# Kernel tuning notes

Measured on AMD Instinct MI355X. Metric: run time of the kernel, lower is better.

## Reference

```python
import jax, jax.numpy as jnp
import numpy as np

D_MODEL = 2048
D_HEAD = 64
Q_HEADS = 32
KV_HEADS = 8


def rope(x):
    # x: [B, S, H, D], rotate interleaved pairs along last dim
    B, S, H, D = x.shape
    pos = jnp.arange(S, dtype=x.dtype)
    freq = 1.0 / (10000.0 ** (jnp.arange(0, D, 2, dtype=x.dtype) / D))  # [D/2]
    theta = pos[:, None] * freq[None, :]                                 # [S, D/2]
    cos = jnp.cos(theta)[None, :, None, :]
    sin = jnp.sin(theta)[None, :, None, :]
    xr = x.reshape(B, S, H, D // 2, 2)
    x1, x2 = xr[..., 0], xr[..., 1]
    out = jnp.stack((x1 * cos - x2 * sin, x1 * sin + x2 * cos), axis=-1)
    return out.reshape(B, S, H, D)


def setup_inputs() -> dict:
    key = jax.random.key(0)
    ks = jax.random.split(key, 7)
    x = jax.random.normal(ks[0], (1, 2048, D_MODEL), dtype=jnp.float32)
    W_q = jax.random.normal(ks[1], (Q_HEADS * D_HEAD, D_MODEL), dtype=jnp.float32) * 0.02
    b_q = jnp.zeros((Q_HEADS * D_HEAD,), dtype=jnp.float32)
    W_kv = jax.random.normal(ks[2], (2 * KV_HEADS * D_HEAD, D_MODEL), dtype=jnp.float32) * 0.02
    b_kv = jnp.zeros((2 * KV_HEADS * D_HEAD,), dtype=jnp.float32)
    W_out = jax.random.normal(ks[3], (D_MODEL, D_MODEL), dtype=jnp.float32) * 0.02
    b_out = jnp.zeros((D_MODEL,), dtype=jnp.float32)
    return {"x": x, "W_q": W_q, "b_q": b_q, "W_kv": W_kv, "b_kv": b_kv,
            "W_out": W_out, "b_out": b_out}


def reference(x, W_q, b_q, W_kv, b_kv, W_out, b_out):
    B, S, _ = x.shape
    g = Q_HEADS // KV_HEADS
    Q = (x @ W_q.T + b_q).reshape(B, S, Q_HEADS, D_HEAD)
    kv = x @ W_kv.T + b_kv
    K, V = jnp.split(kv, 2, axis=-1)
    K = K.reshape(B, S, KV_HEADS, D_HEAD)
    V = V.reshape(B, S, KV_HEADS, D_HEAD)
    Q = rope(Q)
    K = rope(K)
    K = jnp.repeat(K, g, axis=2)  # [B, S, Q_HEADS, D_HEAD]
    V = jnp.repeat(V, g, axis=2)
    scale = 1.0 / (D_HEAD ** 0.5)
    scores = jnp.einsum('bqhd,bkhd->bhqk', Q, K) * scale  # [B,H,S,S]
    # note: original calls non-inplace masked_fill and discards it, so no causal mask applied
    probs = jax.nn.softmax(scores, axis=-1)
    attn = jnp.einsum('bhqk,bkhd->bqhd', probs, V).reshape(B, S, D_MODEL)
    return attn @ W_out.T + b_out
```

## Files before the change

### kernel.cpp

```cpp
#include <hip/hip_runtime.h>
#include <hip/hip_bf16.h>
#include <math.h>

#define S_LEN 2048
#define D_MODEL 2048
#define Q_HEADS 32
#define KV_HEADS 8

typedef __attribute__((ext_vector_type(8))) short short8;
typedef __attribute__((ext_vector_type(4))) float f32x4;

__device__ __forceinline__ short bf16_rne(float f) {
  unsigned u = __float_as_uint(f);
  unsigned r = (u + 0x7FFFu + ((u >> 16) & 1u)) >> 16;
  return (short)r;
}
__device__ __forceinline__ void dma16(const short* g, short* l) {
  __builtin_amdgcn_global_load_lds(
      (const __attribute__((address_space(1))) void*)g,
      (__attribute__((address_space(3))) void*)l, 16, 0, 0);
}
__device__ __forceinline__ void fast_sincos(float theta, float& sn, float& cs) {
  double rev = (double)theta * 0.15915494309189535;
  float fr = (float)(rev - floor(rev));
  sn = __builtin_amdgcn_sinf(fr);
  cs = __builtin_amdgcn_cosf(fr);
}
__device__ __forceinline__ void cvt8(const float* src, short* dst, int i) {
  float4 a = *(const float4*)&src[i];
  float4 b = *(const float4*)&src[i + 4];
  short8 h;
  h[0] = bf16_rne(a.x); h[1] = bf16_rne(a.y);
  h[2] = bf16_rne(a.z); h[3] = bf16_rne(a.w);
  h[4] = bf16_rne(b.x); h[5] = bf16_rne(b.y);
  h[6] = bf16_rne(b.z); h[7] = bf16_rne(b.w);
  *(short8*)&dst[i] = h;
}

#define NM (2048 * 2048)
#define NKV (1024 * 2048)

__global__ __launch_bounds__(256) void cvt_all(
    const float* __restrict__ x,    short* __restrict__ xh,
    const float* __restrict__ wq,   short* __restrict__ wqh,
    const float* __restrict__ wkv,  short* __restrict__ wkvh,
    const float* __restrict__ wo,   short* __restrict__ woh,
    float* __restrict__ freqTab) {
  if (blockIdx.x == 0 && threadIdx.x < 32) {
    const double e = (2.0 * threadIdx.x) / 64.0;
    freqTab[threadIdx.x] = (float)pow(10000.0, -e);
  }
  int i = (blockIdx.x * 256 + threadIdx.x) * 8;
  if (i < NM) { cvt8(x, xh, i); return; }
  i -= NM;
  if (i < NM) { cvt8(wq, wqh, i); return; }
  i -= NM;
  if (i < NKV) { cvt8(wkv, wkvh, i); return; }
  i -= NKV;
  cvt8(wo, woh, i);
}

__global__ __launch_bounds__(256) void gemm_nt1_dual(
    const short* __restrict__ Ah,
    const short* __restrict__ Bq, const short* __restrict__ Bkv,
    const float* __restrict__ bq, const float* __restrict__ bkv,
    float* __restrict__ Cq, float* __restrict__ Ckv,
    int Nq, int Nkv, int K) {
  __shared__ short As[2][128 * 32];
  __shared__ short Bs[2][64 * 32];
  const int tid = threadIdx.x;
  const int w = tid >> 6, lane = tid & 63;
  const int l16 = lane & 15, quad = lane >> 4;
  const int bm = blockIdx.y * 128;
  const int bnG = blockIdx.x * 64;

  const short* Bsrc; const float* bias; float* Cp; int pitch; int bn;
  if (bnG < Nq) { Bsrc = Bq;  bias = bq;  Cp = Cq;  pitch = Nq;  bn = bnG; }
  else          { Bsrc = Bkv; bias = bkv; Cp = Ckv; pitch = Nkv; bn = bnG - Nq; }

  const int drow0 = w * 16 + (lane >> 2);
  const int drow1 = drow0 + 64;
  const int slot = lane & 3;
  const int ch0 = slot ^ ((drow0 >> 1) & 3);
  const int ch1 = slot ^ ((drow1 >> 1) & 3);
  const size_t a0 = (size_t)(bm + drow0) * K + ch0 * 8;
  const size_t a1 = (size_t)(bm + drow1) * K + ch1 * 8;
  const size_t b0 = (size_t)(bn + drow0) * K + ch0 * 8;
  const int dA0 = (w * 16) * 32, dA1 = (64 + w * 16) * 32;

  const int wm = (w & 1) * 64, wn = (w >> 1) * 32;
  int offA[4], offB[2];
#pragma unroll
  for (int i = 0; i < 4; ++i) {
    int R = wm + i * 16 + l16;
    offA[i] = R * 32 + (quad ^ ((R >> 1) & 3)) * 8;
  }
#pragma unroll
  for (int j = 0; j < 2; ++j) {
    int R = wn + j * 16 + l16;
    offB[j] = R * 32 + (quad ^ ((R >> 1) & 3)) * 8;
  }

  f32x4 acc[4][2];
#pragma unroll
  for (int i = 0; i < 4; ++i)
#pragma unroll
    for (int j = 0; j < 2; ++j)
#pragma unroll
      for (int e = 0; e < 4; ++e) acc[i][j][e] = 0.f;

  const int T = K / 32;
  dma16(Ah + a0, &As[0][dA0]);
  dma16(Ah + a1, &As[0][dA1]);
  dma16(Bsrc + b0, &Bs[0][dA0]);
  __syncthreads();

  for (int t = 0; t < T; ++t) {
    const int cur = t & 1, nxt = cur ^ 1;
    if (t + 1 < T) {
      const int ko = (t + 1) * 32;
      dma16(Ah + a0 + ko, &As[nxt][dA0]);
      dma16(Ah + a1 + ko, &As[nxt][dA1]);
      dma16(Bsrc + b0 + ko, &Bs[nxt][dA0]);
    }
    short8 af[4], bf[2];
#pragma unroll
    for (int i = 0; i < 4; ++i) af[i] = *(const short8*)&As[cur][offA[i]];
#pragma unroll
    for (int j = 0; j < 2; ++j) bf[j] = *(const short8*)&Bs[cur][offB[j]];
#pragma unroll
    for (int i = 0; i < 4; ++i)
#pragma unroll
      for (int j = 0; j < 2; ++j)
        acc[i][j] = __builtin_amdgcn_mfma_f32_16x16x32_bf16(af[i], bf[j], acc[i][j], 0, 0, 0);
    __syncthreads();
  }

#pragma unroll
  for (int i = 0; i < 4; ++i) {
#pragma unroll
    for (int j = 0; j < 2; ++j) {
      const int col = bn + wn + j * 16 + l16;
      const float bv = bias[col];
      const int row0 = bm + wm + i * 16 + quad * 4;
#pragma unroll
      for (int e = 0; e < 4; ++e)
        Cp[(size_t)(row0 + e) * pitch + col] = acc[i][j][e] + bv;
    }
  }
}

__global__ __launch_bounds__(256) void gemm_nt1_big(
    const short* __restrict__ A, const short* __restrict__ B,
    const float* __restrict__ bias, float* __restrict__ C,
    int N, int K) {
  __shared__ short As[2][128 * 32];
  __shared__ short Bs[2][128 * 32];
  const int tid = threadIdx.x;
  const int w = tid >> 6, lane = tid & 63;
  const int l16 = lane & 15, quad = lane >> 4;
  const int bm = blockIdx.y * 128;
  const int bn = blockIdx.x * 128;

  const int drow0 = w * 16 + (lane >> 2);
  const int drow1 = drow0 + 64;
  const int slot = lane & 3;
  const int ch0 = slot ^ ((drow0 >> 1) & 3);
  const int ch1 = slot ^ ((drow1 >> 1) & 3);
  const short* gA0 = &A[(size_t)(bm + drow0) * K + ch0 * 8];
  const short* gA1 = &A[(size_t)(bm + drow1) * K + ch1 * 8];
  const short* gB0 = &B[(size_t)(bn + drow0) * K + ch0 * 8];
  const short* gB1 = &B[(size_t)(bn + drow1) * K + ch1 * 8];
  const int dA0 = (w * 16) * 32, dA1 = (64 + w * 16) * 32;

  const int wm = (w & 1) * 64, wn = (w >> 1) * 64;
  int offA[4], offB[4];
#pragma unroll
  for (int i = 0; i < 4; ++i) {
    int R = wm + i * 16 + l16;
    offA[i] = R * 32 + (quad ^ ((R >> 1) & 3)) * 8;
    int Rb = wn + i * 16 + l16;
    offB[i] = Rb * 32 + (quad ^ ((Rb >> 1) & 3)) * 8;
  }

  f32x4 acc[4][4];
#pragma unroll
  for (int i = 0; i < 4; ++i)
#pragma unroll
    for (int j = 0; j < 4; ++j)
#pragma unroll
      for (int e = 0; e < 4; ++e) acc[i][j][e] = 0.f;

  const int T = K / 32;
  dma16(gA0, &As[0][dA0]);
  dma16(gA1, &As[0][dA1]);
  dma16(gB0, &Bs[0][dA0]);
  dma16(gB1, &Bs[0][dA1]);
  __syncthreads();

  for (int t = 0; t < T; ++t) {
    const int cur = t & 1, nxt = cur ^ 1;
    if (t + 1 < T) {
      const int ko = (t + 1) * 32;
      dma16(gA0 + ko, &As[nxt][dA0]);
      dma16(gA1 + ko, &As[nxt][dA1]);
      dma16(gB0 + ko, &Bs[nxt][dA0]);
      dma16(gB1 + ko, &Bs[nxt][dA1]);
    }
    short8 af[4], bf[4];
#pragma unroll
    for (int i = 0; i < 4; ++i) af[i] = *(const short8*)&As[cur][offA[i]];
#pragma unroll
    for (int j = 0; j < 4; ++j) bf[j] = *(const short8*)&Bs[cur][offB[j]];
#pragma unroll
    for (int i = 0; i < 4; ++i)
#pragma unroll
      for (int j = 0; j < 4; ++j)
        acc[i][j] = __builtin_amdgcn_mfma_f32_16x16x32_bf16(af[i], bf[j], acc[i][j], 0, 0, 0);
    __syncthreads();
  }

#pragma unroll
  for (int i = 0; i < 4; ++i) {
#pragma unroll
    for (int j = 0; j < 4; ++j) {
      const int col = bn + wn + j * 16 + l16;
      const float bv = bias[col];
      const int row0 = bm + wm + i * 16 + quad * 4;
#pragma unroll
      for (int e = 0; e < 4; ++e)
        C[(size_t)(row0 + e) * N + col] = acc[i][j][e] + bv;
    }
  }
}

#define QSCALE 0.18033688011112042f

__global__ __launch_bounds__(256) void rope_all(
    const float* __restrict__ Qf, const float* __restrict__ KVf,
    const float* __restrict__ tab, short* __restrict__ Qb,
    short* __restrict__ Kb, short* __restrict__ Vt) {
  __shared__ short Vtile[64][72];
  const int tid = threadIdx.x;

  if (blockIdx.x < 8192) {
    const int g = blockIdx.x * 256 + tid;
    const int s = g >> 10;
    const int rem = g & 1023;
    const int h = rem >> 5, j = rem & 31;
    const float theta = (float)s * tab[j];
    float sn, cs;
    fast_sincos(theta, sn, cs);
    const float* p = &Qf[(size_t)s * D_MODEL + h * 64 + 2 * j];
    const float x1 = p[0], x2 = p[1];
    short2 o;
    o.x = bf16_rne((x1 * cs - x2 * sn) * QSCALE);
    o.y = bf16_rne((x1 * sn + x2 * cs) * QSCALE);
    *(short2*)&Qb[((size_t)h * S_LEN + s) * 64 + 2 * j] = o;
    return;
  }

  const int bb = blockIdx.x - 8192;
  const int st = bb & 31, kvh = bb >> 5;

  {
    const int sr = tid >> 2, sc = (tid & 3) * 16;
    const int s = st * 64 + sr;
    const float* kg = &KVf[(size_t)s * 1024 + kvh * 64 + sc];
    short tmp[16];
#pragma unroll
    for (int i = 0; i < 8; ++i) {
      const int j = (sc >> 1) + i;
      const float theta = (float)s * tab[j];
      float sn, cs;
      fast_sincos(theta, sn, cs);
      const float x1 = kg[2 * i], x2 = kg[2 * i + 1];
      tmp[2 * i]     = bf16_rne(x1 * cs - x2 * sn);
      tmp[2 * i + 1] = bf16_rne(x1 * sn + x2 * cs);
    }
    short* out = &Kb[((size_t)kvh * S_LEN + s) * 64 + sc];
    *(short8*)&out[0] = *(short8*)&tmp[0];
    *(short8*)&out[8] = *(short8*)&tmp[8];
  }

  {
    const int sr = tid >> 2, sc = (tid & 3) * 16;
    const float* vg = &KVf[(size_t)(st * 64 + sr) * 1024 + 512 + kvh * 64 + sc];
    short tmp[16];
#pragma unroll
    for (int c = 0; c < 16; c += 4) {
      float4 v = *(const float4*)&vg[c];
      tmp[c + 0] = bf16_rne(v.x);
      tmp[c + 1] = bf16_rne(v.y);
      tmp[c + 2] = bf16_rne(v.z);
      tmp[c + 3] = bf16_rne(v.w);
    }
    *(short8*)&Vtile[sr][sc]     = *(short8*)&tmp[0];
    *(short8*)&Vtile[sr][sc + 8] = *(short8*)&tmp[8];
  }
  __syncthreads();
  {
    const int d = tid & 63, kchunk = tid >> 6;
    short tmp[16];
#pragma unroll
    for (int k = 0; k < 16; ++k) tmp[k] = Vtile[kchunk * 16 + k][d];
    short* out = &Vt[((size_t)kvh * 64 + d) * S_LEN + st * 64 + kchunk * 16];
    *(short8*)&out[0] = *(short8*)&tmp[0];
    *(short8*)&out[8] = *(short8*)&tmp[8];
  }
}

__global__ __launch_bounds__(256, 4) void flash8(
    const short* __restrict__ Qb, const short* __restrict__ Kb,
    const short* __restrict__ Vt, short* __restrict__ Oh) {
  const int qt = blockIdx.x, h = blockIdx.y;
  const int kvh = h >> 2;
  const int tid = threadIdx.x;
  const int w = tid >> 6, lane = tid & 63;
  const int l16 = lane & 15, quad = lane >> 4;

  __shared__ short Ks[2][64 * 64];
  __shared__ short Vs[2][64 * 64];
  __shared__ short Ps[64 * 64];

  const short* Kh = Kb + (size_t)kvh * S_LEN * 64;
  const short* Vh = Vt + (size_t)kvh * 64 * S_LEN;
  const int qr = qt * 64 + w * 16 + l16;

  short8 qf0 = *(const short8*)&Qb[((size_t)h * S_LEN + qr) * 64 + quad * 8];
  short8 qf1 = *(const short8*)&Qb[((size_t)h * S_LEN + qr) * 64 + 32 + quad * 8];

  short8 ones;
#pragma unroll
  for (int e = 0; e < 8; ++e) ones[e] = (short)0x3F80;

  const int drow = lane >> 3;
  const int ch = (lane & 7) ^ drow;
  const short* gK = &Kh[(size_t)(w * 16 + drow) * 64 + ch * 8];
  const short* gV = &Vh[(size_t)(w * 16 + drow) * S_LEN + ch * 8];

  const int sl0 = quad ^ (l16 & 7);
  int offT[4][2];
#pragma unroll
  for (int m = 0; m < 4; ++m) {
    offT[m][0] = (m * 16 + l16) * 64 + sl0 * 8;
    offT[m][1] = (m * 16 + l16) * 64 + (sl0 ^ 4) * 8;
  }

  const int prow = (w * 16 + l16) * 64;
  const int pswz = (l16 & 7) << 1;
  int pwr[4];
#pragma unroll
  for (int m = 0; m < 4; ++m) pwr[m] = prow + ((4 * m + quad) ^ pswz) * 4;
  const int prd0 = prow + ((2 * quad) ^ pswz) * 4;
  const int prd1 = prow + ((8 + 2 * quad) ^ pswz) * 4;

  f32x4 accl;
#pragma unroll
  for (int e = 0; e < 4; ++e) accl[e] = 0.f;
  f32x4 acco[4];
#pragma unroll
  for (int m = 0; m < 4; ++m)
#pragma unroll
    for (int e = 0; e < 4; ++e) acco[m][e] = 0.f;

  dma16(gK,               &Ks[0][(w * 16) * 64]);
  dma16(gK + 8 * 64,      &Ks[0][(w * 16 + 8) * 64]);
  dma16(gV,               &Vs[0][(w * 16) * 64]);
  dma16(gV + 8 * S_LEN,   &Vs[0][(w * 16 + 8) * 64]);
  __syncthreads();

  for (int t = 0; t < 32; ++t) {
    const int cur = t & 1, nxt = cur ^ 1;
    if (t + 1 < 32) {
      const short* gKn = gK + (t + 1) * 4096;
      const short* gVn = gV + (t + 1) * 64;
      dma16(gKn,             &Ks[nxt][(w * 16) * 64]);
      dma16(gKn + 8 * 64,    &Ks[nxt][(w * 16 + 8) * 64]);
      dma16(gVn,             &Vs[nxt][(w * 16) * 64]);
      dma16(gVn + 8 * S_LEN, &Vs[nxt][(w * 16 + 8) * 64]);
    }

    const short* kc = Ks[cur];
    f32x4 accs[4];
#pragma unroll
    for (int m = 0; m < 4; ++m)
#pragma unroll
      for (int e = 0; e < 4; ++e) accs[m][e] = 0.f;
#pragma unroll
    for (int m = 0; m < 4; ++m) {
      short8 k0 = *(const short8*)&kc[offT[m][0]];
      short8 k1 = *(const short8*)&kc[offT[m][1]];
      accs[m] = __builtin_amdgcn_mfma_f32_16x16x32_bf16(k0, qf0, accs[m], 0, 0, 0);
      accs[m] = __builtin_amdgcn_mfma_f32_16x16x32_bf16(k1, qf1, accs[m], 0, 0, 0);
    }

#pragma unroll
    for (int m = 0; m < 4; ++m) {
      float p0 = exp2f(accs[m][0]);
      float p1 = exp2f(accs[m][1]);
      float p2 = exp2f(accs[m][2]);
      float p3 = exp2f(accs[m][3]);
      unsigned u01 = __builtin_amdgcn_perm(__float_as_uint(p1), __float_as_uint(p0), 0x07060302u);
      unsigned u23 = __builtin_amdgcn_perm(__float_as_uint(p3), __float_as_uint(p2), 0x07060302u);
      *(uint2*)&Ps[pwr[m]] = make_uint2(u01, u23);
    }

    short8 pf0 = *(const short8*)&Ps[prd0];
    short8 pf1 = *(const short8*)&Ps[prd1];
    accl = __builtin_amdgcn_mfma_f32_16x16x32_bf16(ones, pf0, accl, 0, 0, 0);
    accl = __builtin_amdgcn_mfma_f32_16x16x32_bf16(ones, pf1, accl, 0, 0, 0);
    const short* vc = Vs[cur];
#pragma unroll
    for (int m = 0; m < 4; ++m) {
      short8 v0 = *(const short8*)&vc[offT[m][0]];
      short8 v1 = *(const short8*)&vc[offT[m][1]];
      acco[m] = __builtin_amdgcn_mfma_f32_16x16x32_bf16(v0, pf0, acco[m], 0, 0, 0);
      acco[m] = __builtin_amdgcn_mfma_f32_16x16x32_bf16(v1, pf1, acco[m], 0, 0, 0);
    }

    __syncthreads();
  }

  const float inv = 1.f / accl[0];
#pragma unroll
  for (int m = 0; m < 4; ++m) {
    short4 h4;
    h4.x = bf16_rne(acco[m][0] * inv);
    h4.y = bf16_rne(acco[m][1] * inv);
    h4.z = bf16_rne(acco[m][2] * inv);
    h4.w = bf16_rne(acco[m][3] * inv);
    const size_t base = (size_t)qr * D_MODEL + h * 64 + m * 16 + quad * 4;
    *(short4*)&Oh[base] = h4;
  }
}

extern "C" void kernel_launch(void* const* d_in, const int* in_sizes, int n_in,
                              void* d_out, int out_size, void* d_ws, size_t ws_size,
                              hipStream_t stream) {
  const float* x     = (const float*)d_in[0];
  const float* W_q   = (const float*)d_in[1];
  const float* b_q   = (const float*)d_in[2];
  const float* W_kv  = (const float*)d_in[3];
  const float* b_kv  = (const float*)d_in[4];
  const float* W_out = (const float*)d_in[5];
  const float* b_out = (const float*)d_in[6];
  float* out = (float*)d_out;

  char* ws = (char*)d_ws;
  float* Qbuf  = (float*)(ws);
  float* KVbuf = (float*)(ws + (16u << 20));
  short* xh    = (short*)(ws + (24u << 20));
  short* Wqh   = (short*)(ws + (32u << 20));
  short* Wkvh  = (short*)(ws + (40u << 20));
  short* Woh   = (short*)(ws + (44u << 20));
  short* Qb    = (short*)(ws + (52u << 20));
  short* Kb    = (short*)(ws + (60u << 20));
  short* Vtb   = (short*)(ws + (62u << 20));
  float* freqTab = (float*)(ws + (64u << 20));
  short* Ath   = xh;

  cvt_all<<<7168, 256, 0, stream>>>(x, xh, W_q, Wqh, W_kv, Wkvh, W_out, Woh,
                                    freqTab);

  gemm_nt1_dual<<<dim3(3072 / 64, 2048 / 128), 256, 0, stream>>>(
      xh, Wqh, Wkvh, b_q, b_kv, Qbuf, KVbuf, 2048, 1024, 2048);

  rope_all<<<8192 + 256, 256, 0, stream>>>(Qbuf, KVbuf, freqTab, Qb, Kb, Vtb);

  flash8<<<dim3(S_LEN / 64, Q_HEADS), 256, 0, stream>>>(Qb, Kb, Vtb, Ath);

  gemm_nt1_big<<<dim3(2048 / 128, 2048 / 128), 256, 0, stream>>>(
      Ath, Woh, b_out, out, 2048, 2048);
}
```

Baseline: 264.2 us.

## Fuse RoPE, scaling, bf16 cast and V transpose into QKV GEMM epilogue

Removes the separate rope_all kernel and the fp32 Q/KV intermediates by applying RoPE, the Q scale and bf16 rounding directly in the QKV GEMM epilogue. Rotation partners are exchanged with a lane shuffle, and V is written transposed straight from the accumulators. The flash kernel now reads Q and K in row-major [S, heads*64] layout with strided addressing. This saves one launch and a large fp32 write/read round trip, in exchange for scattered short4 and scalar bf16 stores in the epilogue and less contiguous K loads in attention.

Result: no change. 261.7 us (-1.0%).

```diff
diff --git a/kernel.cpp b/kernel.cpp
--- a/kernel.cpp
+++ b/kernel.cpp
@@ -60,12 +60,16 @@
   cvt8(wo, woh, i);
 }
 
-__global__ __launch_bounds__(256) void gemm_nt1_dual(
+#define QSCALE 0.18033688011112042f
+
+__global__ __launch_bounds__(256) void gemm_qkv_rope(
     const short* __restrict__ Ah,
     const short* __restrict__ Bq, const short* __restrict__ Bkv,
     const float* __restrict__ bq, const float* __restrict__ bkv,
-    float* __restrict__ Cq, float* __restrict__ Ckv,
-    int Nq, int Nkv, int K) {
+    const float* __restrict__ tab,
+    short* __restrict__ Qrm, short* __restrict__ Krm,
+    short* __restrict__ Vt) {
+  const int Nq = 2048, K = 2048;
   __shared__ short As[2][128 * 32];
   __shared__ short Bs[2][64 * 32];
   const int tid = threadIdx.x;
@@ -74,9 +78,10 @@
   const int bm = blockIdx.y * 128;
   const int bnG = blockIdx.x * 64;
 
-  const short* Bsrc; const float* bias; float* Cp; int pitch; int bn;
-  if (bnG < Nq) { Bsrc = Bq;  bias = bq;  Cp = Cq;  pitch = Nq;  bn = bnG; }
-  else          { Bsrc = Bkv; bias = bkv; Cp = Ckv; pitch = Nkv; bn = bnG - Nq; }
+  const short* Bsrc; const float* bias; int bn;
+  if (bnG < Nq) { Bsrc = Bq;  bias = bq;  bn = bnG; }
+  else          { Bsrc = Bkv; bias = bkv; bn = bnG - Nq; }
+  const int mode = (bnG < Nq) ? 0 : ((bnG < Nq + 512) ? 1 : 2);
 
   const int drow0 = w * 16 + (lane >> 2);
   const int drow1 = drow0 + 64;
@@ -138,14 +143,35 @@
 
 #pragma unroll
   for (int i = 0; i < 4; ++i) {
+    const int row0 = bm + wm + i * 16 + quad * 4;
 #pragma unroll
     for (int j = 0; j < 2; ++j) {
       const int col = bn + wn + j * 16 + l16;
       const float bv = bias[col];
-      const int row0 = bm + wm + i * 16 + quad * 4;
-#pragma unroll
-      for (int e = 0; e < 4; ++e)
-        Cp[(size_t)(row0 + e) * pitch + col] = acc[i][j][e] + bv;
+      if (mode == 2) {
+        const int d = col - 512;
+        short4 sv;
+        sv.x = bf16_rne(acc[i][j][0] + bv);
+        sv.y = bf16_rne(acc[i][j][1] + bv);
+        sv.z = bf16_rne(acc[i][j][2] + bv);
+        sv.w = bf16_rne(acc[i][j][3] + bv);
+        *(short4*)&Vt[(size_t)d * S_LEN + row0] = sv;
+      } else {
+        const float fr = tab[(col & 63) >> 1];
+        const float sgn = (col & 1) ? 1.f : -1.f;
+#pragma unroll
+        for (int e = 0; e < 4; ++e) {
+          float v = acc[i][j][e] + bv;
+          float other = __shfl_xor(v, 1);
+          float sn, cs;
+          fast_sincos((float)(row0 + e) * fr, sn, cs);
+          const float o = v * cs + sgn * other * sn;
+          if (mode == 0)
+            Qrm[(size_t)(row0 + e) * D_MODEL + col] = bf16_rne(o * QSCALE);
+          else
+            Krm[(size_t)(row0 + e) * 512 + col] = bf16_rne(o);
+        }
+      }
     }
   }
 }
@@ -234,84 +260,8 @@
   }
 }
 
-#define QSCALE 0.18033688011112042f
-
-__global__ __launch_bounds__(256) void rope_all(
-    const float* __restrict__ Qf, const float* __restrict__ KVf,
-    const float* __restrict__ tab, short* __restrict__ Qb,
-    short* __restrict__ Kb, short* __restrict__ Vt) {
-  __shared__ short Vtile[64][72];
-  const int tid = threadIdx.x;
-
-  if (blockIdx.x < 8192) {
-    const int g = blockIdx.x * 256 + tid;
-    const int s = g >> 10;
-    const int rem = g & 1023;
-    const int h = rem >> 5, j = rem & 31;
-    const float theta = (float)s * tab[j];
-    float sn, cs;
-    fast_sincos(theta, sn, cs);
-    const float* p = &Qf[(size_t)s * D_MODEL + h * 64 + 2 * j];
-    const float x1 = p[0], x2 = p[1];
-    short2 o;
-    o.x = bf16_rne((x1 * cs - x2 * sn) * QSCALE);
-    o.y = bf16_rne((x1 * sn + x2 * cs) * QSCALE);
-    *(short2*)&Qb[((size_t)h * S_LEN + s) * 64 + 2 * j] = o;
-    return;
-  }
-
-  const int bb = blockIdx.x - 8192;
-  const int st = bb & 31, kvh = bb >> 5;
-
-  {
-    const int sr = tid >> 2, sc = (tid & 3) * 16;
-    const int s = st * 64 + sr;
-    const float* kg = &KVf[(size_t)s * 1024 + kvh * 64 + sc];
-    short tmp[16];
-#pragma unroll
-    for (int i = 0; i < 8; ++i) {
-      const int j = (sc >> 1) + i;
-      const float theta = (float)s * tab[j];
-      float sn, cs;
-      fast_sincos(theta, sn, cs);
-      const float x1 = kg[2 * i], x2 = kg[2 * i + 1];
-      tmp[2 * i]     = bf16_rne(x1 * cs - x2 * sn);
-      tmp[2 * i + 1] = bf16_rne(x1 * sn + x2 * cs);
-    }
-    short* out = &Kb[((size_t)kvh * S_LEN + s) * 64 + sc];
-    *(short8*)&out[0] = *(short8*)&tmp[0];
-    *(short8*)&out[8] = *(short8*)&tmp[8];
-  }
-
-  {
-    const int sr = tid >> 2, sc = (tid & 3) * 16;
-    const float* vg = &KVf[(size_t)(st * 64 + sr) * 1024 + 512 + kvh * 64 + sc];
-    short tmp[16];
-#pragma unroll
-    for (int c = 0; c < 16; c += 4) {
-      float4 v = *(const float4*)&vg[c];
-      tmp[c + 0] = bf16_rne(v.x);
-      tmp[c + 1] = bf16_rne(v.y);
-      tmp[c + 2] = bf16_rne(v.z);
-      tmp[c + 3] = bf16_rne(v.w);
-    }
-    *(short8*)&Vtile[sr][sc]     = *(short8*)&tmp[0];
-    *(short8*)&Vtile[sr][sc + 8] = *(short8*)&tmp[8];
-  }
-  __syncthreads();
-  {
-    const int d = tid & 63, kchunk = tid >> 6;
-    short tmp[16];
-#pragma unroll
-    for (int k = 0; k < 16; ++k) tmp[k] = Vtile[kchunk * 16 + k][d];
-    short* out = &Vt[((size_t)kvh * 64 + d) * S_LEN + st * 64 + kchunk * 16];
-    *(short8*)&out[0] = *(short8*)&tmp[0];
-    *(short8*)&out[8] = *(short8*)&tmp[8];
-  }
-}
-
 __global__ __launch_bounds__(256, 4) void flash8(
-    const short* __restrict__ Qb, const short* __restrict__ Kb,
+    const short* __restrict__ Qrm, const short* __restrict__ Krm,
     const short* __restrict__ Vt, short* __restrict__ Oh) {
   const int qt = blockIdx.x, h = blockIdx.y;
   const int kvh = h >> 2;
@@ -323,12 +273,11 @@
   __shared__ short Vs[2][64 * 64];
   __shared__ short Ps[64 * 64];
 
-  const short* Kh = Kb + (size_t)kvh * S_LEN * 64;
   const short* Vh = Vt + (size_t)kvh * 64 * S_LEN;
   const int qr = qt * 64 + w * 16 + l16;
 
-  short8 qf0 = *(const short8*)&Qb[((size_t)h * S_LEN + qr) * 64 + quad * 8];
-  short8 qf1 = *(const short8*)&Qb[((size_t)h * S_LEN + qr) * 64 + 32 + quad * 8];
+  short8 qf0 = *(const short8*)&Qrm[(size_t)qr * D_MODEL + h * 64 + quad * 8];
+  short8 qf1 = *(const short8*)&Qrm[(size_t)qr * D_MODEL + h * 64 + 32 + quad * 8];
 
   short8 ones;
 #pragma unroll
@@ -336,7 +285,7 @@
 
   const int drow = lane >> 3;
   const int ch = (lane & 7) ^ drow;
-  const short* gK = &Kh[(size_t)(w * 16 + drow) * 64 + ch * 8];
+  const short* gK = &Krm[(size_t)(w * 16 + drow) * 512 + kvh * 64 + ch * 8];
   const short* gV = &Vh[(size_t)(w * 16 + drow) * S_LEN + ch * 8];
 
   const int sl0 = quad ^ (l16 & 7);
@@ -365,7 +314,7 @@
     for (int e = 0; e < 4; ++e) acco[m][e] = 0.f;
 
   dma16(gK,               &Ks[0][(w * 16) * 64]);
-  dma16(gK + 8 * 64,      &Ks[0][(w * 16 + 8) * 64]);
+  dma16(gK + 8 * 512,     &Ks[0][(w * 16 + 8) * 64]);
   dma16(gV,               &Vs[0][(w * 16) * 64]);
   dma16(gV + 8 * S_LEN,   &Vs[0][(w * 16 + 8) * 64]);
   __syncthreads();
@@ -373,10 +322,10 @@
   for (int t = 0; t < 32; ++t) {
     const int cur = t & 1, nxt = cur ^ 1;
     if (t + 1 < 32) {
-      const short* gKn = gK + (t + 1) * 4096;
+      const short* gKn = gK + (size_t)(t + 1) * 64 * 512;
       const short* gVn = gV + (t + 1) * 64;
       dma16(gKn,             &Ks[nxt][(w * 16) * 64]);
-      dma16(gKn + 8 * 64,    &Ks[nxt][(w * 16 + 8) * 64]);
+      dma16(gKn + 8 * 512,   &Ks[nxt][(w * 16 + 8) * 64]);
       dma16(gVn,             &Vs[nxt][(w * 16) * 64]);
       dma16(gVn + 8 * S_LEN, &Vs[nxt][(w * 16 + 8) * 64]);
     }
@@ -448,27 +397,23 @@
   float* out = (float*)d_out;
 
   char* ws = (char*)d_ws;
-  float* Qbuf  = (float*)(ws);
-  float* KVbuf = (float*)(ws + (16u << 20));
-  short* xh    = (short*)(ws + (24u << 20));
-  short* Wqh   = (short*)(ws + (32u << 20));
-  short* Wkvh  = (short*)(ws + (40u << 20));
-  short* Woh   = (short*)(ws + (44u << 20));
-  short* Qb    = (short*)(ws + (52u << 20));
-  short* Kb    = (short*)(ws + (60u << 20));
-  short* Vtb   = (short*)(ws + (62u << 20));
-  float* freqTab = (float*)(ws + (64u << 20));
+  short* xh    = (short*)(ws);
+  short* Wqh   = (short*)(ws + (8u << 20));
+  short* Wkvh  = (short*)(ws + (16u << 20));
+  short* Woh   = (short*)(ws + (20u << 20));
+  short* Qrm   = (short*)(ws + (28u << 20));
+  short* Krm   = (short*)(ws + (36u << 20));
+  short* Vtb   = (short*)(ws + (38u << 20));
+  float* freqTab = (float*)(ws + (40u << 20));
   short* Ath   = xh;
 
   cvt_all<<<7168, 256, 0, stream>>>(x, xh, W_q, Wqh, W_kv, Wkvh, W_out, Woh,
                                     freqTab);
 
-  gemm_nt1_dual<<<dim3(3072 / 64, 2048 / 128), 256, 0, stream>>>(
-      xh, Wqh, Wkvh, b_q, b_kv, Qbuf, KVbuf, 2048, 1024, 2048);
-
-  rope_all<<<8192 + 256, 256, 0, stream>>>(Qbuf, KVbuf, freqTab, Qb, Kb, Vtb);
-
-  flash8<<<dim3(S_LEN / 64, Q_HEADS), 256, 0, stream>>>(Qb, Kb, Vtb, Ath);
+  gemm_qkv_rope<<<dim3(3072 / 64, 2048 / 128), 256, 0, stream>>>(
+      xh, Wqh, Wkvh, b_q, b_kv, freqTab, Qrm, Krm, Vtb);
+
+  flash8<<<dim3(S_LEN / 64, Q_HEADS), 256, 0, stream>>>(Qrm, Krm, Vtb, Ath);
 
   gemm_nt1_big<<<dim3(2048 / 128, 2048 / 128), 256, 0, stream>>>(
       Ath, Woh, b_out, out, 2048, 2048);
```
